# Optimization experiments

Measured on AMD Instinct MI355X. Metric: run time of the kernel, lower is better.

Reference implementation:

```python
import jax, jax.numpy as jnp
import numpy as np

N = 100000
F_IN = 128
F_OUT = 128
NNZ = 1_600_000  # avg degree 16


def spmm(rows, cols, vals, X, n):
    """Sparse [n,n] (COO: rows, cols, vals) times dense X [n,d] -> [n,d]."""
    return jax.ops.segment_sum(vals[:, None] * X[cols], rows, num_segments=n)


def setup_inputs() -> dict:
    key = jax.random.key(0)
    ks = jax.random.split(key, 8)
    x = jax.random.normal(ks[0], (N, F_IN), dtype=jnp.float32)
    W = jax.random.normal(ks[1], (F_IN, F_OUT), dtype=jnp.float32) * 0.05
    kernel = jnp.ones((N, 1), dtype=jnp.float32)  # tf.ones_initializer
    phi0_rows = jax.random.randint(ks[2], (NNZ,), 0, N, dtype=jnp.int64)
    phi0_cols = jax.random.randint(ks[3], (NNZ,), 0, N, dtype=jnp.int64)
    phi0_vals = jax.random.uniform(ks[4], (NNZ,), dtype=jnp.float32)
    phi1_rows = jax.random.randint(ks[5], (NNZ,), 0, N, dtype=jnp.int64)
    phi1_cols = jax.random.randint(ks[6], (NNZ,), 0, N, dtype=jnp.int64)
    phi1_vals = jax.random.uniform(ks[7], (NNZ,), dtype=jnp.float32)
    return {
        "x": x, "W": W, "kernel": kernel,
        "phi0_rows": phi0_rows, "phi0_cols": phi0_cols, "phi0_vals": phi0_vals,
        "phi1_rows": phi1_rows, "phi1_cols": phi1_cols, "phi1_vals": phi1_vals,
    }


def reference(x, W, kernel, phi0_rows, phi0_cols, phi0_vals,
              phi1_rows, phi1_cols, phi1_vals):
    # X' = x @ W  (dense feature projection)
    X_prime = x @ W  # [N, F_OUT]
    # X'_t = phi0 @ X'  (SpMM with wavelet basis)
    X_t = spmm(phi0_rows, phi0_cols, phi0_vals, X_prime, N)
    # out = phi1 @ (kernel * X'_t)  (elementwise spectral scaling then SpMM)
    out = spmm(phi1_rows, phi1_cols, phi1_vals, kernel * X_t, N)
    return jax.nn.relu(out)
```

## Files before the change

kernel.cpp:

```cpp
#include <hip/hip_runtime.h>


constexpr int kN = 100000;
constexpr int kF = 128;
constexpr int kNNZ = 1600000;

constexpr int kBuckets = (kN + 127) / 128;
constexpr int kBucketCap = 2432;
constexpr int kChunk = 4096;
constexpr int kChunkBlocks = (kNNZ + kChunk - 1) / kChunk;
constexpr int kScatBlocks = 2 * kChunkBlocks;
constexpr int kGemmBlocks = (kN + 63) / 64;

typedef short bf16x8 __attribute__((ext_vector_type(8)));
typedef float f32x4 __attribute__((ext_vector_type(4)));
typedef unsigned short ushort4v __attribute__((ext_vector_type(4)));

__device__ __forceinline__ unsigned short f32_to_bf16(float f) {
    unsigned int u = __float_as_uint(f);
    u += 0x7fffu + ((u >> 16) & 1u);
    return (unsigned short)(u >> 16);
}
__device__ __forceinline__ float bf16_to_f32(unsigned short h) {
    return __uint_as_float((unsigned int)h << 16);
}

__global__ __launch_bounds__(256) void transpose_w(const float* __restrict__ W,
                                                   unsigned short* __restrict__ Wt,
                                                   int* __restrict__ g0,
                                                   int* __restrict__ g1) {
    const int t = threadIdx.x;
    const int e = blockIdx.x * 256 + t;
    const int n = e & 127, k = e >> 7;
    Wt[n * 128 + k] = f32_to_bf16(W[e]);
    if (blockIdx.x == 0) {
        for (int i = t; i < kBuckets; i += 256) {
            g0[i] = i * kBucketCap;
            g1[i] = i * kBucketCap;
        }
    }
}

__global__ __launch_bounds__(256) void fused_gemm_scatter(
    const float* __restrict__ x, const unsigned short* __restrict__ Wt,
    unsigned short* __restrict__ Xpb,
    const int* __restrict__ r0, const int* __restrict__ c0, const float* __restrict__ v0,
    const int* __restrict__ r1, const int* __restrict__ c1, const float* __restrict__ v1,
    int* __restrict__ gc0, int* __restrict__ gc1,
    unsigned long long* __restrict__ s0, unsigned long long* __restrict__ s1) {
    __shared__ __align__(16) char smem[kChunk * 4 + 2 * kBuckets * 4];
    const int t = threadIdx.x;

    if (blockIdx.x >= kScatBlocks) {
        unsigned short* xs = (unsigned short*)smem;
        const int rowBase = (blockIdx.x - kScatBlocks) * 64;

        {
            const int lrow = t >> 2;
            const int q = t & 3;
            int srow = rowBase + lrow;
            if (srow >= kN) srow = kN - 1;
            const float4* xr = (const float4*)(x + (size_t)srow * kF) + q * 8;
            #pragma unroll
            for (int i = 0; i < 8; ++i) {
                const float4 f = xr[i];
                ushort4v h;
                h.x = f32_to_bf16(f.x); h.y = f32_to_bf16(f.y);
                h.z = f32_to_bf16(f.z); h.w = f32_to_bf16(f.w);
                const int kidx = q * 32 + i * 4;
                *(ushort4v*)&xs[lrow * 128 + (kidx ^ ((lrow & 7) << 3))] = h;
            }
        }
        __syncthreads();

        const int w = t >> 6;
        const int l = t & 63;
        const int lr = l & 15;
        const int lq = l >> 4;

        f32x4 acc[8];
        #pragma unroll
        for (int n = 0; n < 8; ++n) acc[n] = (f32x4){0.f, 0.f, 0.f, 0.f};

        const int arow = w * 16 + lr;
        #pragma unroll
        for (int ks = 0; ks < 4; ++ks) {
            const int akidx = ks * 32 + lq * 8;
            const bf16x8 a = *(const bf16x8*)&xs[arow * 128 + (akidx ^ ((arow & 7) << 3))];
            #pragma unroll
            for (int n = 0; n < 8; ++n) {
                const int bn = n * 16 + lr;
                const bf16x8 b = *(const bf16x8*)(Wt + bn * 128 + akidx);
                acc[n] = __builtin_amdgcn_mfma_f32_16x16x32_bf16(a, b, acc[n], 0, 0, 0);
            }
        }

        #pragma unroll
        for (int j = 0; j < 4; ++j) {
            const int row = rowBase + w * 16 + lq * 4 + j;
            if (row < kN) {
                unsigned short* orow = Xpb + (size_t)row * kF + lr;
                #pragma unroll
                for (int n = 0; n < 8; ++n) orow[n * 16] = f32_to_bf16(acc[n][j]);
            }
        }
    } else {
        int* rowsc = (int*)smem;
        int* hist  = rowsc + kChunk;
        int* hbase = hist + kBuckets;
        const int b = blockIdx.x;
        const bool m1 = b >= kChunkBlocks;
        const int cb = m1 ? b - kChunkBlocks : b;
        const int* rows = m1 ? r1 : r0;
        const int* cols = m1 ? c1 : c0;
        const float* vals = m1 ? v1 : v0;
        int* gcur = m1 ? gc1 : gc0;
        unsigned long long* stg = m1 ? s1 : s0;

        for (int i = t; i < kBuckets; i += 256) hist[i] = 0;
        __syncthreads();

        const int base0 = cb * kChunk;
        for (int j = 0; j < kChunk; j += 256) {
            const int idx = base0 + j + t;
            const int r = (idx < kNNZ) ? rows[idx] : -1;
            rowsc[j + t] = r;
            if (r >= 0) atomicAdd(&hist[r >> 7], 1);
        }
        __syncthreads();

        for (int i = t; i < kBuckets; i += 256) {
            const int c = hist[i];
            hbase[i] = c ? atomicAdd(&gcur[i], c) : 0;
            hist[i] = 0;
        }
        __syncthreads();

        for (int j = 0; j < kChunk; j += 256) {
            const int idx = base0 + j + t;
            const int r = rowsc[j + t];
            if (r >= 0) {
                const int bk = r >> 7;
                const int pos = hbase[bk] + atomicAdd(&hist[bk], 1);
                const unsigned int key =
                    ((unsigned int)(r & 127) << 17) | (unsigned int)cols[idx];
                stg[pos] = ((unsigned long long)__float_as_uint(vals[idx]) << 32) | key;
            }
        }
    }
}

template <bool ROW_SCALE, bool RELU, bool OUT_BF16>
__global__ __launch_bounds__(256) void sort_spmm(const int* __restrict__ gcur,
                                                 const unsigned long long* __restrict__ stg,
                                                 const float* __restrict__ scale,
                                                 const unsigned short* __restrict__ Xin,
                                                 void* __restrict__ Xout) {
    __shared__ unsigned long long recs[kBucketCap];
    __shared__ int hist[128];
    __shared__ int sc[128];
    __shared__ int cur[128];

    const int bk = blockIdx.x;
    const int t = threadIdx.x;
    const int start = bk * kBucketCap;
    const int nrec = gcur[bk] - start;

    if (t < 128) hist[t] = 0;
    __syncthreads();

    for (int i = t; i < nrec; i += 256) {
        const unsigned int lo = (unsigned int)stg[start + i];
        atomicAdd(&hist[(lo >> 17) & 127], 1);
    }
    __syncthreads();

    const int v = (t < 128) ? hist[t] : 0;
    if (t < 128) sc[t] = v;
    __syncthreads();
    #pragma unroll
    for (int off = 1; off < 128; off <<= 1) {
        const int add = (t < 128 && t >= off) ? sc[t - off] : 0;
        __syncthreads();
        if (t < 128) sc[t] += add;
        __syncthreads();
    }
    if (t < 128) cur[t] = sc[t] - v;
    __syncthreads();

    for (int i = t; i < nrec; i += 256) {
        const unsigned long long p = stg[start + i];
        const int lr = (int)(((unsigned int)p >> 17) & 127);
        recs[atomicAdd(&cur[lr], 1)] = p;
    }
    __syncthreads();

    const int rg = t >> 5;
    const int lane = t & 31;
    for (int i = 0; i < 16; ++i) {
        const int lr = rg * 16 + i;
        const int row = bk * 128 + lr;
        if (row >= kN) continue;
        const int e = sc[lr];
        const int s = e - hist[lr];

        float4 acc = make_float4(0.f, 0.f, 0.f, 0.f);
        int j = s;
        for (; j + 4 <= e; j += 4) {
            const unsigned long long p0 = recs[j];
            const unsigned long long p1 = recs[j + 1];
            const unsigned long long p2 = recs[j + 2];
            const unsigned long long p3 = recs[j + 3];
            const int cc0 = (int)((unsigned int)p0 & 0x1FFFF);
            const int cc1 = (int)((unsigned int)p1 & 0x1FFFF);
            const int cc2 = (int)((unsigned int)p2 & 0x1FFFF);
            const int cc3 = (int)((unsigned int)p3 & 0x1FFFF);
            const float w0 = __uint_as_float((unsigned int)(p0 >> 32));
            const float w1 = __uint_as_float((unsigned int)(p1 >> 32));
            const float w2 = __uint_as_float((unsigned int)(p2 >> 32));
            const float w3 = __uint_as_float((unsigned int)(p3 >> 32));
            const ushort4v x0 = *(const ushort4v*)(Xin + (size_t)cc0 * kF + lane * 4);
            const ushort4v x1 = *(const ushort4v*)(Xin + (size_t)cc1 * kF + lane * 4);
            const ushort4v x2 = *(const ushort4v*)(Xin + (size_t)cc2 * kF + lane * 4);
            const ushort4v x3 = *(const ushort4v*)(Xin + (size_t)cc3 * kF + lane * 4);
            acc.x = fmaf(w0, bf16_to_f32(x0.x), acc.x);
            acc.y = fmaf(w0, bf16_to_f32(x0.y), acc.y);
            acc.z = fmaf(w0, bf16_to_f32(x0.z), acc.z);
            acc.w = fmaf(w0, bf16_to_f32(x0.w), acc.w);
            acc.x = fmaf(w1, bf16_to_f32(x1.x), acc.x);
            acc.y = fmaf(w1, bf16_to_f32(x1.y), acc.y);
            acc.z = fmaf(w1, bf16_to_f32(x1.z), acc.z);
            acc.w = fmaf(w1, bf16_to_f32(x1.w), acc.w);
            acc.x = fmaf(w2, bf16_to_f32(x2.x), acc.x);
            acc.y = fmaf(w2, bf16_to_f32(x2.y), acc.y);
            acc.z = fmaf(w2, bf16_to_f32(x2.z), acc.z);
            acc.w = fmaf(w2, bf16_to_f32(x2.w), acc.w);
            acc.x = fmaf(w3, bf16_to_f32(x3.x), acc.x);
            acc.y = fmaf(w3, bf16_to_f32(x3.y), acc.y);
            acc.z = fmaf(w3, bf16_to_f32(x3.z), acc.z);
            acc.w = fmaf(w3, bf16_to_f32(x3.w), acc.w);
        }
        for (; j < e; ++j) {
            const unsigned long long p = recs[j];
            const int cc = (int)((unsigned int)p & 0x1FFFF);
            const float wv = __uint_as_float((unsigned int)(p >> 32));
            const ushort4v xv = *(const ushort4v*)(Xin + (size_t)cc * kF + lane * 4);
            acc.x = fmaf(wv, bf16_to_f32(xv.x), acc.x);
            acc.y = fmaf(wv, bf16_to_f32(xv.y), acc.y);
            acc.z = fmaf(wv, bf16_to_f32(xv.z), acc.z);
            acc.w = fmaf(wv, bf16_to_f32(xv.w), acc.w);
        }

        if (ROW_SCALE) {
            const float k = scale[row];
            acc.x *= k; acc.y *= k; acc.z *= k; acc.w *= k;
        }
        if (RELU) {
            acc.x = fmaxf(acc.x, 0.f); acc.y = fmaxf(acc.y, 0.f);
            acc.z = fmaxf(acc.z, 0.f); acc.w = fmaxf(acc.w, 0.f);
        }
        if (OUT_BF16) {
            ushort4v o;
            o.x = f32_to_bf16(acc.x); o.y = f32_to_bf16(acc.y);
            o.z = f32_to_bf16(acc.z); o.w = f32_to_bf16(acc.w);
            *(ushort4v*)((unsigned short*)Xout + (size_t)row * kF + lane * 4) = o;
        } else {
            ((float4*)Xout)[(size_t)row * 32 + lane] = acc;
        }
    }
}

extern "C" void kernel_launch(void* const* d_in, const int* in_sizes, int n_in,
                              void* d_out, int out_size, void* d_ws, size_t ws_size,
                              hipStream_t stream) {
    const float* x    = (const float*)d_in[0];
    const float* W    = (const float*)d_in[1];
    const float* kern = (const float*)d_in[2];
    const int*   p0r  = (const int*)d_in[3];
    const int*   p0c  = (const int*)d_in[4];
    const float* p0v  = (const float*)d_in[5];
    const int*   p1r  = (const int*)d_in[6];
    const int*   p1c  = (const int*)d_in[7];
    const float* p1v  = (const float*)d_in[8];
    float* out = (float*)d_out;

    char* w = (char*)d_ws;
    size_t off = 0;
    unsigned short* Xpb = (unsigned short*)(w + off); off += (size_t)kN * kF * 2;
    unsigned short* Xtb = (unsigned short*)(w + off); off += (size_t)kN * kF * 2;
    unsigned short* Wt = (unsigned short*)(w + off);  off += 128 * 128 * 2;
    int* gcur0 = (int*)(w + off);                     off += 4096;
    int* gcur1 = (int*)(w + off);                     off += 4096;
    unsigned long long* stg0 = (unsigned long long*)(w + off);
    off += (size_t)kBuckets * kBucketCap * 8;
    unsigned long long* stg1 = (unsigned long long*)(w + off);
    off += (size_t)kBuckets * kBucketCap * 8;

    transpose_w<<<64, 256, 0, stream>>>(W, Wt, gcur0, gcur1);

    fused_gemm_scatter<<<kScatBlocks + kGemmBlocks, 256, 0, stream>>>(
        x, Wt, Xpb, p0r, p0c, p0v, p1r, p1c, p1v, gcur0, gcur1, stg0, stg1);

    sort_spmm<true, false, true><<<kBuckets, 256, 0, stream>>>(
        gcur0, stg0, kern, Xpb, Xtb);

    sort_spmm<false, true, false><<<kBuckets, 256, 0, stream>>>(
        gcur1, stg1, nullptr, Xtb, out);
}
```

Before: 224.0 us.

## Replace global-atomic bucket scatter with per-chunk local sort and directory

Each scatter block now sorts its chunk into 256-row buckets locally in shared memory, writes the records contiguously, and records per-bucket offsets in a per-chunk directory. The SpMM blocks (now 512 threads, 256 rows each) gather their bucket's segments from every chunk. This removes global atomics on bucket cursors and the fixed-capacity staging, and the GEMM is split back out of the fused scatter kernel. In exchange, each SpMM block reads many short segments (one per chunk), which is scattered, lower-efficiency memory access, and the fused GEMM/scatter overlap is lost.

```diff
diff --git a/kernel.cpp b/kernel.cpp
--- a/kernel.cpp
+++ b/kernel.cpp
@@ -5,11 +5,12 @@
 constexpr int kF = 128;
 constexpr int kNNZ = 1600000;
 
-constexpr int kBuckets = (kN + 127) / 128;
-constexpr int kBucketCap = 2432;
-constexpr int kChunk = 4096;
+constexpr int kBuckets = (kN + 255) / 256;
+constexpr int kBucketCap = 4608;
+constexpr int kChunk = 7168;
 constexpr int kChunkBlocks = (kNNZ + kChunk - 1) / kChunk;
-constexpr int kScatBlocks = 2 * kChunkBlocks;
+constexpr int kSlotsPerMat = kChunkBlocks * kChunk;
+constexpr int kDirStride = kBuckets + 1;
 constexpr int kGemmBlocks = (kN + 63) / 64;
 
 typedef short bf16x8 __attribute__((ext_vector_type(8)));
@@ -26,191 +27,213 @@
 }
 
 __global__ __launch_bounds__(256) void transpose_w(const float* __restrict__ W,
-                                                   unsigned short* __restrict__ Wt,
-                                                   int* __restrict__ g0,
-                                                   int* __restrict__ g1) {
-    const int t = threadIdx.x;
-    const int e = blockIdx.x * 256 + t;
+                                                   unsigned short* __restrict__ Wt) {
+    const int e = blockIdx.x * 256 + threadIdx.x;
     const int n = e & 127, k = e >> 7;
     Wt[n * 128 + k] = f32_to_bf16(W[e]);
-    if (blockIdx.x == 0) {
-        for (int i = t; i < kBuckets; i += 256) {
-            g0[i] = i * kBucketCap;
-            g1[i] = i * kBucketCap;
-        }
-    }
-}
-
-__global__ __launch_bounds__(256) void fused_gemm_scatter(
-    const float* __restrict__ x, const unsigned short* __restrict__ Wt,
-    unsigned short* __restrict__ Xpb,
+}
+
+__global__ __launch_bounds__(256) void gemm_mfma(const float* __restrict__ x,
+                                                 const unsigned short* __restrict__ Wt,
+                                                 unsigned short* __restrict__ Xpb) {
+    __shared__ __align__(16) unsigned short xs[64 * 128];
+    const int t = threadIdx.x;
+    const int rowBase = blockIdx.x * 64;
+
+    {
+        const int lrow = t >> 2;
+        const int q = t & 3;
+        int srow = rowBase + lrow;
+        if (srow >= kN) srow = kN - 1;
+        const float4* xr = (const float4*)(x + (size_t)srow * kF) + q * 8;
+        #pragma unroll
+        for (int i = 0; i < 8; ++i) {
+            const float4 f = xr[i];
+            ushort4v h;
+            h.x = f32_to_bf16(f.x); h.y = f32_to_bf16(f.y);
+            h.z = f32_to_bf16(f.z); h.w = f32_to_bf16(f.w);
+            const int kidx = q * 32 + i * 4;
+            *(ushort4v*)&xs[lrow * 128 + (kidx ^ ((lrow & 7) << 3))] = h;
+        }
+    }
+    __syncthreads();
+
+    const int w = t >> 6;
+    const int l = t & 63;
+    const int lr = l & 15;
+    const int lq = l >> 4;
+
+    f32x4 acc[8];
+    #pragma unroll
+    for (int n = 0; n < 8; ++n) acc[n] = (f32x4){0.f, 0.f, 0.f, 0.f};
+
+    const int arow = w * 16 + lr;
+    #pragma unroll
+    for (int ks = 0; ks < 4; ++ks) {
+        const int akidx = ks * 32 + lq * 8;
+        const bf16x8 a = *(const bf16x8*)&xs[arow * 128 + (akidx ^ ((arow & 7) << 3))];
+        #pragma unroll
+        for (int n = 0; n < 8; ++n) {
+            const int bn = n * 16 + lr;
+            const bf16x8 b = *(const bf16x8*)(Wt + bn * 128 + akidx);
+            acc[n] = __builtin_amdgcn_mfma_f32_16x16x32_bf16(a, b, acc[n], 0, 0, 0);
+        }
+    }
+
+    #pragma unroll
+    for (int j = 0; j < 4; ++j) {
+        const int row = rowBase + w * 16 + lq * 4 + j;
+        if (row < kN) {
+            unsigned short* orow = Xpb + (size_t)row * kF + lr;
+            #pragma unroll
+            for (int n = 0; n < 8; ++n) orow[n * 16] = f32_to_bf16(acc[n][j]);
+        }
+    }
+}
+
+__global__ __launch_bounds__(256) void bucket_scatter(
     const int* __restrict__ r0, const int* __restrict__ c0, const float* __restrict__ v0,
     const int* __restrict__ r1, const int* __restrict__ c1, const float* __restrict__ v1,
-    int* __restrict__ gc0, int* __restrict__ gc1,
-    unsigned long long* __restrict__ s0, unsigned long long* __restrict__ s1) {
-    __shared__ __align__(16) char smem[kChunk * 4 + 2 * kBuckets * 4];
+    unsigned long long* __restrict__ stg, unsigned short* __restrict__ dir) {
+    __shared__ unsigned long long recs[kChunk];
+    __shared__ int hist[kDirStride];
+    __shared__ int loff[kDirStride];
+    __shared__ int cur[kDirStride];
+    __shared__ int sc2[256];
+
+    const int b = blockIdx.x;
+    const bool m1 = b >= kChunkBlocks;
+    const int cb = m1 ? b - kChunkBlocks : b;
+    const int* rows = m1 ? r1 : r0;
+    const int* cols = m1 ? c1 : c0;
+    const float* vals = m1 ? v1 : v0;
+    unsigned long long* dst = stg + (size_t)b * kChunk;
+    unsigned short* dirm = dir + (size_t)b * kDirStride;
+
     const int t = threadIdx.x;
-
-    if (blockIdx.x >= kScatBlocks) {
-        unsigned short* xs = (unsigned short*)smem;
-        const int rowBase = (blockIdx.x - kScatBlocks) * 64;
-
-        {
-            const int lrow = t >> 2;
-            const int q = t & 3;
-            int srow = rowBase + lrow;
-            if (srow >= kN) srow = kN - 1;
-            const float4* xr = (const float4*)(x + (size_t)srow * kF) + q * 8;
-            #pragma unroll
-            for (int i = 0; i < 8; ++i) {
-                const float4 f = xr[i];
-                ushort4v h;
-                h.x = f32_to_bf16(f.x); h.y = f32_to_bf16(f.y);
-                h.z = f32_to_bf16(f.z); h.w = f32_to_bf16(f.w);
-                const int kidx = q * 32 + i * 4;
-                *(ushort4v*)&xs[lrow * 128 + (kidx ^ ((lrow & 7) << 3))] = h;
-            }
-        }
+    for (int i = t; i < kDirStride; i += 256) hist[i] = 0;
+    __syncthreads();
+
+    const int base0 = cb * kChunk;
+    for (int j = t; j < kChunk; j += 256) {
+        const int idx = base0 + j;
+        if (idx < kNNZ) atomicAdd(&hist[rows[idx] >> 8], 1);
+    }
+    __syncthreads();
+
+    int s = 0;
+    if (t < 196) s = hist[2 * t] + hist[2 * t + 1];
+    sc2[t] = (t < 196) ? s : 0;
+    __syncthreads();
+    #pragma unroll
+    for (int off = 1; off < 256; off <<= 1) {
+        const int add = (t >= off) ? sc2[t - off] : 0;
         __syncthreads();
-
-        const int w = t >> 6;
-        const int l = t & 63;
-        const int lr = l & 15;
-        const int lq = l >> 4;
-
-        f32x4 acc[8];
-        #pragma unroll
-        for (int n = 0; n < 8; ++n) acc[n] = (f32x4){0.f, 0.f, 0.f, 0.f};
-
-        const int arow = w * 16 + lr;
-        #pragma unroll
-        for (int ks = 0; ks < 4; ++ks) {
-            const int akidx = ks * 32 + lq * 8;
-            const bf16x8 a = *(const bf16x8*)&xs[arow * 128 + (akidx ^ ((arow & 7) << 3))];
-            #pragma unroll
-            for (int n = 0; n < 8; ++n) {
-                const int bn = n * 16 + lr;
-                const bf16x8 b = *(const bf16x8*)(Wt + bn * 128 + akidx);
-                acc[n] = __builtin_amdgcn_mfma_f32_16x16x32_bf16(a, b, acc[n], 0, 0, 0);
-            }
-        }
-
-        #pragma unroll
-        for (int j = 0; j < 4; ++j) {
-            const int row = rowBase + w * 16 + lq * 4 + j;
-            if (row < kN) {
-                unsigned short* orow = Xpb + (size_t)row * kF + lr;
-                #pragma unroll
-                for (int n = 0; n < 8; ++n) orow[n * 16] = f32_to_bf16(acc[n][j]);
-            }
-        }
-    } else {
-        int* rowsc = (int*)smem;
-        int* hist  = rowsc + kChunk;
-        int* hbase = hist + kBuckets;
-        const int b = blockIdx.x;
-        const bool m1 = b >= kChunkBlocks;
-        const int cb = m1 ? b - kChunkBlocks : b;
-        const int* rows = m1 ? r1 : r0;
-        const int* cols = m1 ? c1 : c0;
-        const float* vals = m1 ? v1 : v0;
-        int* gcur = m1 ? gc1 : gc0;
-        unsigned long long* stg = m1 ? s1 : s0;
-
-        for (int i = t; i < kBuckets; i += 256) hist[i] = 0;
+        sc2[t] += add;
         __syncthreads();
-
-        const int base0 = cb * kChunk;
-        for (int j = 0; j < kChunk; j += 256) {
-            const int idx = base0 + j + t;
-            const int r = (idx < kNNZ) ? rows[idx] : -1;
-            rowsc[j + t] = r;
-            if (r >= 0) atomicAdd(&hist[r >> 7], 1);
-        }
-        __syncthreads();
-
-        for (int i = t; i < kBuckets; i += 256) {
-            const int c = hist[i];
-            hbase[i] = c ? atomicAdd(&gcur[i], c) : 0;
-            hist[i] = 0;
-        }
-        __syncthreads();
-
-        for (int j = 0; j < kChunk; j += 256) {
-            const int idx = base0 + j + t;
-            const int r = rowsc[j + t];
-            if (r >= 0) {
-                const int bk = r >> 7;
-                const int pos = hbase[bk] + atomicAdd(&hist[bk], 1);
-                const unsigned int key =
-                    ((unsigned int)(r & 127) << 17) | (unsigned int)cols[idx];
-                stg[pos] = ((unsigned long long)__float_as_uint(vals[idx]) << 32) | key;
-            }
-        }
-    }
+    }
+    if (t < 196) {
+        const int ex = sc2[t] - s;
+        loff[2 * t] = ex;             loff[2 * t + 1] = ex + hist[2 * t];
+        cur[2 * t] = ex;              cur[2 * t + 1] = ex + hist[2 * t];
+        dirm[2 * t] = (unsigned short)ex;
+        dirm[2 * t + 1] = (unsigned short)(ex + hist[2 * t]);
+    }
+    __syncthreads();
+
+    for (int j = t; j < kChunk; j += 256) {
+        const int idx = base0 + j;
+        if (idx < kNNZ) {
+            const int r = rows[idx];
+            const int bk = r >> 8;
+            const int pos = atomicAdd(&cur[bk], 1);
+            const unsigned int key =
+                ((unsigned int)(r & 255) << 17) | (unsigned int)cols[idx];
+            recs[pos] = ((unsigned long long)__float_as_uint(vals[idx]) << 32) | key;
+        }
+    }
+    __syncthreads();
+
+    for (int j = t; j < kChunk; j += 256) dst[j] = recs[j];
 }
 
 template <bool ROW_SCALE, bool RELU, bool OUT_BF16>
-__global__ __launch_bounds__(256) void sort_spmm(const int* __restrict__ gcur,
-                                                 const unsigned long long* __restrict__ stg,
-                                                 const float* __restrict__ scale,
-                                                 const unsigned short* __restrict__ Xin,
-                                                 void* __restrict__ Xout) {
-    __shared__ unsigned long long recs[kBucketCap];
-    __shared__ int hist[128];
-    __shared__ int sc[128];
-    __shared__ int cur[128];
+__global__ __launch_bounds__(512) void sort_spmm(
+    const unsigned long long* __restrict__ stg,
+    const unsigned short* __restrict__ dir,
+    const float* __restrict__ scale,
+    const unsigned short* __restrict__ Xin,
+    void* __restrict__ Xout) {
+    __shared__ unsigned long long sorted[kBucketCap];
+    __shared__ int rlen[kChunkBlocks];
+    __shared__ int gst[kChunkBlocks];
+    __shared__ int hist[256];
+    __shared__ int sc[256];
+    __shared__ int cur[256];
 
     const int bk = blockIdx.x;
     const int t = threadIdx.x;
-    const int start = bk * kBucketCap;
-    const int nrec = gcur[bk] - start;
-
-    if (t < 128) hist[t] = 0;
-    __syncthreads();
-
-    for (int i = t; i < nrec; i += 256) {
-        const unsigned int lo = (unsigned int)stg[start + i];
-        atomicAdd(&hist[(lo >> 17) & 127], 1);
-    }
-    __syncthreads();
-
-    const int v = (t < 128) ? hist[t] : 0;
-    if (t < 128) sc[t] = v;
-    __syncthreads();
-    #pragma unroll
-    for (int off = 1; off < 128; off <<= 1) {
-        const int add = (t < 128 && t >= off) ? sc[t - off] : 0;
+
+    if (t < kChunkBlocks) {
+        const unsigned short* dd = dir + (size_t)t * kDirStride;
+        const int s = dd[bk];
+        rlen[t] = dd[bk + 1] - s;
+        gst[t] = t * kChunk + s;
+    }
+    if (t < 256) hist[t] = 0;
+    __syncthreads();
+
+    const int g = t >> 5;
+    const int lane = t & 31;
+
+    for (int blk = g; blk < kChunkBlocks; blk += 16) {
+        const int len = rlen[blk];
+        const int gs = gst[blk];
+        for (int i = lane; i < len; i += 32) {
+            const unsigned int lo = (unsigned int)stg[gs + i];
+            atomicAdd(&hist[(lo >> 17) & 255], 1);
+        }
+    }
+    __syncthreads();
+
+    const int v = (t < 256) ? hist[t] : 0;
+    if (t < 256) sc[t] = v;
+    __syncthreads();
+    #pragma unroll
+    for (int off = 1; off < 256; off <<= 1) {
+        const int add = (t < 256 && t >= off) ? sc[t - off] : 0;
         __syncthreads();
-        if (t < 128) sc[t] += add;
+        if (t < 256) sc[t] += add;
         __syncthreads();
     }
-    if (t < 128) cur[t] = sc[t] - v;
-    __syncthreads();
-
-    for (int i = t; i < nrec; i += 256) {
-        const unsigned long long p = stg[start + i];
-        const int lr = (int)(((unsigned int)p >> 17) & 127);
-        recs[atomicAdd(&cur[lr], 1)] = p;
-    }
-    __syncthreads();
-
-    const int rg = t >> 5;
-    const int lane = t & 31;
+    if (t < 256) cur[t] = sc[t] - v;
+    __syncthreads();
+
+    for (int blk = g; blk < kChunkBlocks; blk += 16) {
+        const int len = rlen[blk];
+        const int gs = gst[blk];
+        for (int i = lane; i < len; i += 32) {
+            const unsigned long long p = stg[gs + i];
+            const int lr = (int)(((unsigned int)p >> 17) & 255);
+            sorted[atomicAdd(&cur[lr], 1)] = p;
+        }
+    }
+    __syncthreads();
+
     for (int i = 0; i < 16; ++i) {
-        const int lr = rg * 16 + i;
-        const int row = bk * 128 + lr;
+        const int lr = g * 16 + i;
+        const int row = bk * 256 + lr;
         if (row >= kN) continue;
         const int e = sc[lr];
-        const int s = e - hist[lr];
+        const int s0 = e - hist[lr];
 
         float4 acc = make_float4(0.f, 0.f, 0.f, 0.f);
-        int j = s;
+        int j = s0;
         for (; j + 4 <= e; j += 4) {
-            const unsigned long long p0 = recs[j];
-            const unsigned long long p1 = recs[j + 1];
-            const unsigned long long p2 = recs[j + 2];
-            const unsigned long long p3 = recs[j + 3];
+            const unsigned long long p0 = sorted[j];
+            const unsigned long long p1 = sorted[j + 1];
+            const unsigned long long p2 = sorted[j + 2];
+            const unsigned long long p3 = sorted[j + 3];
             const int cc0 = (int)((unsigned int)p0 & 0x1FFFF);
             const int cc1 = (int)((unsigned int)p1 & 0x1FFFF);
             const int cc2 = (int)((unsigned int)p2 & 0x1FFFF);
@@ -241,7 +264,7 @@
             acc.w = fmaf(w3, bf16_to_f32(x3.w), acc.w);
         }
         for (; j < e; ++j) {
-            const unsigned long long p = recs[j];
+            const unsigned long long p = sorted[j];
             const int cc = (int)((unsigned int)p & 0x1FFFF);
             const float wv = __uint_as_float((unsigned int)(p >> 32));
             const ushort4v xv = *(const ushort4v*)(Xin + (size_t)cc * kF + lane * 4);
@@ -289,21 +312,24 @@
     unsigned short* Xpb = (unsigned short*)(w + off); off += (size_t)kN * kF * 2;
     unsigned short* Xtb = (unsigned short*)(w + off); off += (size_t)kN * kF * 2;
     unsigned short* Wt = (unsigned short*)(w + off);  off += 128 * 128 * 2;
-    int* gcur0 = (int*)(w + off);                     off += 4096;
-    int* gcur1 = (int*)(w + off);                     off += 4096;
-    unsigned long long* stg0 = (unsigned long long*)(w + off);
-    off += (size_t)kBuckets * kBucketCap * 8;
-    unsigned long long* stg1 = (unsigned long long*)(w + off);
-    off += (size_t)kBuckets * kBucketCap * 8;
-
-    transpose_w<<<64, 256, 0, stream>>>(W, Wt, gcur0, gcur1);
-
-    fused_gemm_scatter<<<kScatBlocks + kGemmBlocks, 256, 0, stream>>>(
-        x, Wt, Xpb, p0r, p0c, p0v, p1r, p1c, p1v, gcur0, gcur1, stg0, stg1);
-
-    sort_spmm<true, false, true><<<kBuckets, 256, 0, stream>>>(
-        gcur0, stg0, kern, Xpb, Xtb);
-
-    sort_spmm<false, true, false><<<kBuckets, 256, 0, stream>>>(
-        gcur1, stg1, nullptr, Xtb, out);
-}
+    unsigned long long* stg = (unsigned long long*)(w + off);
+    off += (size_t)2 * kSlotsPerMat * 8;
+    unsigned short* dir = (unsigned short*)(w + off);
+    off += (size_t)2 * kChunkBlocks * kDirStride * 2;
+
+    const unsigned long long* stg1 = stg + kSlotsPerMat;
+    const unsigned short* dir1 = dir + (size_t)kChunkBlocks * kDirStride;
+
+    transpose_w<<<64, 256, 0, stream>>>(W, Wt);
+
+    gemm_mfma<<<kGemmBlocks, 256, 0, stream>>>(x, Wt, Xpb);
+
+    bucket_scatter<<<2 * kChunkBlocks, 256, 0, stream>>>(
+        p0r, p0c, p0v, p1r, p1c, p1v, stg, dir);
+
+    sort_spmm<true, false, true><<<kBuckets, 512, 0, stream>>>(
+        stg, dir, kern, Xpb, Xtb);
+
+    sort_spmm<false, true, false><<<kBuckets, 512, 0, stream>>>(
+        stg1, dir1, nullptr, Xtb, out);
+}
```

Result: slower. 232.1 us (+3.6%).
